# Performance work log

Measured on AMD Instinct MI355X. Metric: run time of the kernel, lower is better.

The kernel has to match this reference:

```python
import jax, jax.numpy as jnp
import numpy as np

# GNB per-element parameters [s, beta, R, C6] indexed by atomic number Z (rows not listed stay zero)
_ROWS = {
 1:[0.2772,1.7504,3.6516,95.99], 2:[0.2425,2.087,2.1843,40.67], 3:[0.3266,2.3073,1.2711,70.21],
 4:[0.3964,2.8811,3.3497,114.51], 5:[0.3121,2.6366,2.7079,152.36], 6:[0.2455,3.0189,1.8219,184.28],
 7:[0.2743,2.9432,2.4667,482.54], 8:[0.2577,2.7407,2.365,405.57], 9:[0.2791,2.5863,1.5062,218.45],
 10:[0.2378,2.5307,1.8233,174.81], 11:[0.2592,2.5679,1.3974,181.7], 12:[0.3837,2.9613,3.3515,263.02],
 13:[0.3013,3.2377,3.0102,228.1], 14:[0.3202,3.2749,3.1629,359.43], 15:[0.3399,3.7491,3.2554,3222.12],
 16:[0.3215,3.6718,2.9539,2144.49], 17:[0.3071,3.418,3.0368,2072.46], 18:[0.2752,3.3306,2.6598,1357.42],
 19:[0.2264,2.9736,4.0877,1406.65], 20:[0.4015,3.4464,4.1275,1058.36], 21:[0.9388,4.5955,9.7282,11498.73],
 22:[0.6048,3.5334,8.5322,3361.33], 23:[0.3678,3.068,7.2344,2095.91], 24:[0.2848,2.8393,5.3605,1049.31],
 25:[0.355,3.055,3.718,966.27], 26:[0.4406,3.2628,3.6408,1571.36], 27:[0.4124,3.2622,3.4961,1183.59],
 28:[0.3139,2.749,3.5108,787.76], 29:[0.3345,2.9097,3.0537,563.93], 30:[0.3391,2.9024,3.0261,592.91],
 31:[0.3146,3.3924,3.1735,430.82], 32:[0.3327,3.2804,3.1773,812.57], 33:[0.404,3.8757,3.8357,4533.53],
 34:[0.3343,3.8562,3.1109,3440.92], 35:[0.3242,3.7067,3.2122,3859.82], 36:[0.292,3.6457,2.8263,2729.6],
 37:[0.2677,3.4421,2.412,1864.19], 38:[0.3446,3.559,1.894,1175.73], 39:[1.0038,5.7293,11.2061,32141.18],
 40:[0.6146,5.075,6.821,27655.14], 41:[0.4244,3.7156,7.2367,2864.2], 42:[0.4882,3.6853,3.901,3563.45],
 43:[0.4439,3.6987,4.0857,3266.43], 44:[0.4736,3.7826,4.045,3967.23], 45:[0.4039,3.4706,3.4813,2233.82],
 46:[0.3188,3.3433,3.0487,1393.49], 47:[0.2948,3.1186,2.7795,1315.09], 48:[0.3012,3.0853,2.8673,1311.47],
 49:[0.3351,3.5452,3.3339,1460.56], 50:[0.3134,3.2997,3.0086,1662.99], 51:[0.4081,4.1277,3.9919,8089.97],
 52:[0.3585,4.1795,3.4209,6887.05], 53:[0.3574,4.0988,3.5649,8799.32], 54:[0.3134,4.0387,3.0288,6136.5],
 55:[0.2872,3.8468,2.262,3757.31], 56:[0.3788,4.0368,1.3837,2561.18], 57:[1.0851,6.1365,12.171,66580.83],
 72:[0.5577,5.213,6.0791,27593.76], 73:[0.5308,4.7637,5.7661,15364.65], 74:[0.3926,3.6018,3.6366,2734.5],
 75:[0.5351,3.9552,4.241,4801.82], 76:[0.4701,4.0278,4.1348,5685.94], 77:[0.3661,3.6123,3.4213,2786.0],
 78:[0.3411,3.6066,3.2486,2699.79], 79:[0.3164,3.3822,2.9588,2282.6], 80:[0.3047,3.375,2.9381,2476.79],
 81:[0.2802,3.3964,2.7711,2988.7], 82:[0.2682,3.2481,2.5816,2506.63], 83:[0.3876,4.1225,3.785,8916.84],
 84:[0.3679,4.2313,3.5381,8694.22], 85:[0.368,4.2455,3.6985,11821.61], 86:[0.3195,4.1784,3.0551,8410.64],
}
_TAB = np.zeros((87, 4), np.float32)
for _z, _v in _ROWS.items():
    _TAB[_z] = _v
GNB_TABLE = jnp.asarray(_TAB)
C_SP2 = jnp.asarray(np.array([0.2808, 3.0548, 2.2348, 429.69], np.float32))
C_SP3 = jnp.asarray(np.array([0.2455, 3.0189, 1.8219, 184.28], np.float32))
N_CN2 = jnp.asarray(np.array([0.2996, 3.02, 2.6454, 720.18], np.float32))
N_CN3 = jnp.asarray(np.array([0.2743, 2.9432, 2.4667, 482.54], np.float32))

BJ_A1, BJ_A2, BJ_ALPHA = 0.4, 4.0, 14.0
CUTOFF_LR, CUTOFF_START = 10.0, 8.0  # cutoff_start = cutoff_lr - 2.0


def _poly_envelope(x):
    # PolynomialCutoff.calculate_envelope with r_max=1, p=6:
    x6 = x ** 6
    env = 1.0 - 28.0 * x6 + 48.0 * x6 * x - 21.0 * x6 * x * x
    return env * (x < 1.0)


def _gnb_forward(lengths, Z, edge_index):
    n_nodes = Z.shape[0]
    sender, receiver = edge_index[0], edge_index[1]

    # coordination numbers via scatter-add on receiver
    cn = jnp.zeros((n_nodes,), jnp.int32).at[receiver].add(1)

    # species-indexed params with CN-adaptive selection for C and N
    params = GNB_TABLE[Z]  # [N, 4]
    c_params = jnp.where((cn <= 3)[:, None], C_SP2[None, :], C_SP3[None, :])
    n_params = jnp.where((cn <= 2)[:, None], N_CN2[None, :], N_CN3[None, :])
    params = jnp.where((Z == 6)[:, None], c_params, params)
    params = jnp.where((Z == 7)[:, None], n_params, params)

    R_i = params[:, 2]
    C6_i = params[:, 3]

    # geometric-mean combination rules per edge
    C6_ij = jnp.sqrt(C6_i[sender] * C6_i[receiver])
    R_ij = jnp.sqrt(R_i[sender] * R_i[receiver])

    r = lengths
    # BJ damping: f = 1 / (1 + 6 (r/r0)^(-alpha)), r0 = a1 sqrt(R_ij) + a2
    r0 = BJ_A1 * jnp.sqrt(R_ij) + BJ_A2
    f_damp = 1.0 / (1.0 + 6.0 * (r0 / r) ** BJ_ALPHA)

    e_edge = -C6_ij / (R_ij ** 6 + r ** 6) * f_damp

    # long-range polynomial cutoff switching from 1 at cutoff_start to 0 at cutoff_lr
    x = (r - CUTOFF_START) / (CUTOFF_LR - CUTOFF_START)
    env = jnp.where(r < CUTOFF_START, 1.0, _poly_envelope(x))
    e_edge = e_edge * env

    # scatter-sum to atoms; 0.5 to split symmetric pair energy over both directions
    node_energy = jnp.zeros((n_nodes,), e_edge.dtype).at[receiver].add(0.5 * e_edge)
    return node_energy


def setup_inputs() -> dict:
    key = jax.random.key(0)
    k1, k2, k3 = jax.random.split(key, 3)
    n_nodes, n_edges = 100000, 6400000
    Z = jax.random.randint(k1, (n_nodes,), 1, 87, dtype=jnp.int32)
    edge_index = jax.random.randint(k2, (2, n_edges), 0, n_nodes, dtype=jnp.int32)
    lengths = jax.random.uniform(k3, (n_edges,), jnp.float32, 1.0, 10.5)
    return {"Z": Z, "edge_index": edge_index, "lengths": lengths}


def reference(Z, edge_index, lengths):
    return _gnb_forward(lengths, Z, edge_index)
```

## Files before the change

### kernel.cpp

```cpp
#include <hip/hip_runtime.h>


#define B2SHIFT 10
#define B2SIZE  1024
#define TILE    4096
#define SBLK    512
#define ESLICES 32
#define MAXB    128
#define EB      256
#define AREP    4

__device__ __constant__ float2 GNB_RC6[87] = {
    {0.f, 0.f},
    {3.6516f, 95.99f},   {2.1843f, 40.67f},   {1.2711f, 70.21f},
    {3.3497f, 114.51f},  {2.7079f, 152.36f},  {1.8219f, 184.28f},
    {2.4667f, 482.54f},  {2.365f, 405.57f},   {1.5062f, 218.45f},
    {1.8233f, 174.81f},  {1.3974f, 181.7f},   {3.3515f, 263.02f},
    {3.0102f, 228.1f},   {3.1629f, 359.43f},  {3.2554f, 3222.12f},
    {2.9539f, 2144.49f}, {3.0368f, 2072.46f}, {2.6598f, 1357.42f},
    {4.0877f, 1406.65f}, {4.1275f, 1058.36f}, {9.7282f, 11498.73f},
    {8.5322f, 3361.33f}, {7.2344f, 2095.91f}, {5.3605f, 1049.31f},
    {3.718f, 966.27f},   {3.6408f, 1571.36f}, {3.4961f, 1183.59f},
    {3.5108f, 787.76f},  {3.0537f, 563.93f},  {3.0261f, 592.91f},
    {3.1735f, 430.82f},  {3.1773f, 812.57f},  {3.8357f, 4533.53f},
    {3.1109f, 3440.92f}, {3.2122f, 3859.82f}, {2.8263f, 2729.6f},
    {2.412f, 1864.19f},  {1.894f, 1175.73f},  {11.2061f, 32141.18f},
    {6.821f, 27655.14f}, {7.2367f, 2864.2f},  {3.901f, 3563.45f},
    {4.0857f, 3266.43f}, {4.045f, 3967.23f},  {3.4813f, 2233.82f},
    {3.0487f, 1393.49f}, {2.7795f, 1315.09f}, {2.8673f, 1311.47f},
    {3.3339f, 1460.56f}, {3.0086f, 1662.99f}, {3.9919f, 8089.97f},
    {3.4209f, 6887.05f}, {3.5649f, 8799.32f}, {3.0288f, 6136.5f},
    {2.262f, 3757.31f},  {1.3837f, 2561.18f}, {12.171f, 66580.83f},
    {0.f,0.f},{0.f,0.f},{0.f,0.f},{0.f,0.f},{0.f,0.f},{0.f,0.f},{0.f,0.f},
    {0.f,0.f},{0.f,0.f},{0.f,0.f},{0.f,0.f},{0.f,0.f},{0.f,0.f},{0.f,0.f},
    {6.0791f, 27593.76f}, {5.7661f, 15364.65f}, {3.6366f, 2734.5f},
    {4.241f, 4801.82f},   {4.1348f, 5685.94f},  {3.4213f, 2786.0f},
    {3.2486f, 2699.79f},  {2.9588f, 2282.6f},   {2.9381f, 2476.79f},
    {2.7711f, 2988.7f},   {2.5816f, 2506.63f},  {3.785f, 8916.84f},
    {3.5381f, 8694.22f},  {3.6985f, 11821.61f}, {3.0551f, 8410.64f},
};

__global__ void gnb_init(const int* __restrict__ Z, unsigned* __restrict__ isCN,
                         int nw, int n_nodes, int4* __restrict__ zp4, int zq,
                         int* __restrict__ zp, int zwords) {
    int stride = gridDim.x * blockDim.x;
    int t0 = blockIdx.x * blockDim.x + threadIdx.x;
    int4 z4 = make_int4(0, 0, 0, 0);
    for (int i = t0; i < zq; i += stride) zp4[i] = z4;
    for (int i = zq * 4 + t0; i < zwords; i += stride) zp[i] = 0;
    for (int w = t0; w < nw; w += stride) {
        unsigned m = 0;
        int base = w << 5;
        int lim = n_nodes - base; if (lim > 32) lim = 32;
        for (int k = 0; k < lim; ++k) {
            int z = Z[base + k];
            if (z == 6 || z == 7) m |= (1u << k);
        }
        isCN[w] = m;
    }
}

__global__ void __launch_bounds__(EB)
gnb_degree(const int* __restrict__ recv, const unsigned* __restrict__ isCN,
           int* __restrict__ cn, int n_edges) {
    int base = (blockIdx.x * EB + threadIdx.x) * 4;
    if (base + 3 < n_edges) {
        int4 rv = *(const int4*)(recv + base);
        int rr[4] = {rv.x, rv.y, rv.z, rv.w};
        #pragma unroll
        for (int j = 0; j < 4; ++j) {
            unsigned r = (unsigned)rr[j];
            if ((isCN[r >> 5] >> (r & 31)) & 1u) atomicAdd(&cn[r], 1);
        }
    } else {
        for (int j = 0; j < 4; ++j) {
            int e = base + j;
            if (e < n_edges) {
                unsigned r = (unsigned)recv[e];
                if ((isCN[r >> 5] >> (r & 31)) & 1u) atomicAdd(&cn[r], 1);
            }
        }
    }
}

__global__ void gnb_params(const int* __restrict__ Z, const int* __restrict__ cn,
                           float2* __restrict__ P2, int n_nodes) {
    int i = blockIdx.x * blockDim.x + threadIdx.x;
    if (i >= n_nodes) return;
    int z = Z[i];
    float Rp, C6;
    if (z == 6) {
        if (cn[i] <= 3) { Rp = 2.2348f; C6 = 429.69f; }
        else            { Rp = 1.8219f; C6 = 184.28f; }
    } else if (z == 7) {
        if (cn[i] <= 2) { Rp = 2.6454f; C6 = 720.18f; }
        else            { Rp = 2.4667f; C6 = 482.54f; }
    } else {
        float2 rc = GNB_RC6[z];
        Rp = rc.x; C6 = rc.y;
    }
    P2[i] = make_float2(sqrtf(C6), sqrtf(sqrtf(Rp)));
}

__device__ __forceinline__ float gnb_energy_eval(float2 ps, float2 pr, float rlen) {
    float env;
    if (rlen < 8.0f) {
        env = 1.0f;
    } else {
        float x = (rlen - 8.0f) * 0.5f;
        float x2 = x * x;
        float x6 = x2 * x2 * x2;
        env = 1.0f - 28.0f * x6 + 48.0f * x6 * x - 21.0f * x6 * x2;
    }
    float sR  = ps.y * pr.y;
    float C6  = ps.x * pr.x;
    float Rij = sR * sR;
    float R3  = Rij * Rij * Rij;
    float R6  = R3 * R3;
    float r0  = 0.4f * sR + 4.0f;
    float t   = r0 / rlen;
    float t2 = t * t, t4 = t2 * t2, t8 = t4 * t4;
    float t14 = t8 * t4 * t2;
    float fd = 1.0f / (1.0f + 6.0f * t14);
    float rl2 = rlen * rlen;
    float r6 = rl2 * rl2 * rl2;
    return -0.5f * C6 / (R6 + r6) * fd * env;
}

__global__ void __launch_bounds__(SBLK)
gnb_scatter(const int* __restrict__ send, const int* __restrict__ recv,
            const float* __restrict__ len, const float2* __restrict__ P2,
            unsigned* __restrict__ buckets, unsigned* __restrict__ cursor,
            uint2* __restrict__ ovrec, unsigned* __restrict__ ocur,
            int n_edges, unsigned cap, unsigned ocap) {
    __shared__ unsigned hist[MAXB];
    __shared__ unsigned gbase[MAXB];
    const int tid = threadIdx.x;
    const int e0  = blockIdx.x * TILE;

    if (tid < MAXB) hist[tid] = 0;
    __syncthreads();

    unsigned pk[2][4];
    unsigned bk[2][4];
    const bool full = (e0 + TILE <= n_edges);
    #pragma unroll
    for (int k = 0; k < 2; ++k) {
        int base = e0 + (k * SBLK + tid) * 4;
        int ss[4]; int rr[4]; float ll[4];
        if (full) {
            int4   sv = *(const int4*)(send + base);
            int4   rv = *(const int4*)(recv + base);
            float4 lv = *(const float4*)(len + base);
            ss[0]=sv.x; ss[1]=sv.y; ss[2]=sv.z; ss[3]=sv.w;
            rr[0]=rv.x; rr[1]=rv.y; rr[2]=rv.z; rr[3]=rv.w;
            ll[0]=lv.x; ll[1]=lv.y; ll[2]=lv.z; ll[3]=lv.w;
        } else {
            for (int j = 0; j < 4; ++j) {
                int e = base + j;
                bool ok = (e < n_edges);
                ss[j] = ok ? send[e] : 0;
                rr[j] = ok ? recv[e] : 0;
                ll[j] = ok ? len[e]  : 1.0e9f;
            }
        }
        #pragma unroll
        for (int j = 0; j < 4; ++j) {
            if (ll[j] < 10.0f) {
                float e = gnb_energy_eval(P2[ss[j]], P2[rr[j]], ll[j]);
                unsigned eb = (__float_as_uint(e) + 512u) & ~1023u;
                unsigned r  = (unsigned)rr[j];
                unsigned b  = r >> B2SHIFT;
                unsigned off = atomicAdd(&hist[b], 1u);
                pk[k][j] = eb | (r & (B2SIZE - 1));
                bk[k][j] = b | (off << 7);
            } else {
                bk[k][j] = 0xFFFFFFFFu;
            }
        }
    }
    __syncthreads();

    if (tid < MAXB) {
        unsigned c = hist[tid];
        gbase[tid] = c ? atomicAdd(&cursor[tid], c) : 0u;
    }
    __syncthreads();

    #pragma unroll
    for (int k = 0; k < 2; ++k) {
        #pragma unroll
        for (int j = 0; j < 4; ++j) {
            unsigned bo = bk[k][j];
            if (bo != 0xFFFFFFFFu) {
                unsigned b = bo & (MAXB - 1);
                unsigned g = gbase[b] + (bo >> 7);
                if (g < cap) {
                    buckets[(size_t)b * cap + g] = pk[k][j];
                } else {
                    unsigned o = atomicAdd(ocur, 1u);
                    if (o < ocap)
                        ovrec[o] = make_uint2((b << B2SHIFT) | (pk[k][j] & (B2SIZE - 1)),
                                              pk[k][j] & ~1023u);
                }
            }
        }
    }
}

__global__ void __launch_bounds__(256)
gnb_accum(const unsigned* __restrict__ buckets, const unsigned* __restrict__ cursor,
          const uint2* __restrict__ ovrec, const unsigned* __restrict__ ocur,
          float* __restrict__ rep, unsigned cap, unsigned ocap) {
    __shared__ float acc[AREP][B2SIZE + 8];
    const int b   = blockIdx.x / ESLICES;
    const int sl  = blockIdx.x % ESLICES;
    const int tid = threadIdx.x;
    const int rr  = (tid >> 6) & (AREP - 1);

    for (int i = tid; i < AREP * (B2SIZE + 8); i += 256) acc[0][i] = 0.0f;
    __syncthreads();

    unsigned count = cursor[b];
    if (count > cap) count = cap;
    unsigned seg = (((count + ESLICES - 1) / ESLICES) + 3u) & ~3u;
    unsigned st  = (unsigned)sl * seg; if (st > count) st = count;
    unsigned en  = st + seg; if (en > count) en = count;

    const unsigned* src = buckets + (size_t)b * cap;
    for (unsigned i = st + tid * 4; i < en; i += 1024) {
        if (i + 4 <= en) {
            uint4 v = *(const uint4*)(src + i);
            atomicAdd(&acc[rr][v.x & (B2SIZE - 1)], __uint_as_float(v.x & ~1023u));
            atomicAdd(&acc[rr][v.y & (B2SIZE - 1)], __uint_as_float(v.y & ~1023u));
            atomicAdd(&acc[rr][v.z & (B2SIZE - 1)], __uint_as_float(v.z & ~1023u));
            atomicAdd(&acc[rr][v.w & (B2SIZE - 1)], __uint_as_float(v.w & ~1023u));
        } else {
            for (unsigned t = i; t < en; ++t) {
                unsigned v = src[t];
                atomicAdd(&acc[rr][v & (B2SIZE - 1)], __uint_as_float(v & ~1023u));
            }
        }
    }

    if (sl == 0) {
        unsigned n = *ocur; if (n > ocap) n = ocap;
        for (unsigned i = tid; i < n; i += 256) {
            uint2 rc = ovrec[i];
            if ((rc.x >> B2SHIFT) == (unsigned)b)
                atomicAdd(&acc[rr][rc.x & (B2SIZE - 1)], __uint_as_float(rc.y));
        }
    }
    __syncthreads();

    float* dst = rep + (size_t)blockIdx.x * B2SIZE;
    for (int i = tid; i < B2SIZE; i += 256)
        dst[i] = (acc[0][i] + acc[1][i]) + (acc[2][i] + acc[3][i]);
}

__global__ void gnb_reduce(const float* __restrict__ rep, float* __restrict__ out,
                           int n_nodes) {
    int i = blockIdx.x * blockDim.x + threadIdx.x;
    if (i >= n_nodes) return;
    int b = i >> B2SHIFT;
    int j = i & (B2SIZE - 1);
    const float* src = rep + ((size_t)b * ESLICES) * B2SIZE + j;
    float sum = 0.0f;
    #pragma unroll
    for (int s = 0; s < ESLICES; ++s) sum += src[(size_t)s * B2SIZE];
    out[i] = sum;
}

extern "C" void kernel_launch(void* const* d_in, const int* in_sizes, int n_in,
                              void* d_out, int out_size, void* d_ws, size_t ws_size,
                              hipStream_t stream) {
    const int*   Z    = (const int*)d_in[0];
    const int*   eidx = (const int*)d_in[1];
    const float* len  = (const float*)d_in[2];
    float*       out  = (float*)d_out;

    const int n_nodes = in_sizes[0];
    const int n_edges = in_sizes[2];
    const int* send = eidx;
    const int* recv = eidx + n_edges;

    const int NB2 = (n_nodes + B2SIZE - 1) >> B2SHIFT;
    const int nw  = (n_nodes + 31) >> 5;
    const int nwp = (nw + 7) & ~7;

    char* ws = (char*)d_ws;
    unsigned* cursor = (unsigned*)ws;
    unsigned* ocur   = (unsigned*)(ws + MAXB * 4);
    int*      cn     = (int*)(ws + (MAXB + 8) * 4);
    float2*   P2     = (float2*)(ws + ((size_t)n_nodes + MAXB + 8) * 4);
    unsigned* isCN   = (unsigned*)(ws + ((size_t)3 * n_nodes + MAXB + 8) * 4);
    float*    rep    = (float*)((char*)isCN + (size_t)nwp * 4);
    size_t rep_w     = (size_t)NB2 * ESLICES * B2SIZE;
    char*     tail   = (char*)rep + rep_w * 4;

    size_t fixed_words = (size_t)3 * n_nodes + MAXB + 8 + nwp + rep_w;
    size_t total_words = ws_size / 4;
    size_t avail = total_words > fixed_words ? total_words - fixed_words : 0;
    size_t ovw = avail / 64;
    unsigned ocap = (unsigned)((ovw / 2) & ~1ull);
    size_t capw = (avail - ovw) / (size_t)NB2;
    capw &= ~(size_t)3;
    long cap = (long)capw;
    if (cap > n_edges) cap = (n_edges + 3) & ~3;
    if (cap < 0) cap = 0;
    uint2*    ovrec   = (uint2*)tail;
    unsigned* buckets = (unsigned*)(tail + (size_t)ocap * 8);

    const int B = 256;
    int node_blocks = (n_nodes + B - 1) / B;
    int edge4_blocks = (n_edges + EB * 4 - 1) / (EB * 4);
    int scat_blocks = (n_edges + TILE - 1) / TILE;
    int zero_words  = n_nodes + MAXB + 8;
    int zq = zero_words / 4;

    gnb_init<<<256, B, 0, stream>>>(Z, isCN, nw, n_nodes, (int4*)ws, zq,
                                    (int*)ws, zero_words);
    gnb_degree<<<edge4_blocks, EB, 0, stream>>>(recv, isCN, cn, n_edges);
    gnb_params<<<node_blocks, B, 0, stream>>>(Z, cn, P2, n_nodes);
    gnb_scatter<<<scat_blocks, SBLK, 0, stream>>>(send, recv, len, P2, buckets,
                                                  cursor, ovrec, ocur, n_edges,
                                                  (unsigned)cap, ocap);
    gnb_accum<<<NB2 * ESLICES, B, 0, stream>>>(buckets, cursor, ovrec, ocur,
                                               rep, (unsigned)cap, ocap);
    gnb_reduce<<<node_blocks, B, 0, stream>>>(rep, out, n_nodes);
}
```

Before: 232.2 us.

## Batch parameter gathers and defer energy eval past histogram barrier; reduce accum slices

The scatter kernel now loads all eight edges' index and length data up front and issues all sixteen parameter gathers together. It builds the shared-memory histogram first and computes the energies between the global cursor atomic and the barrier, so that math overlaps atomic latency. The receiver's low bits are packed into the bucket key so the packed record is built only at write time. Separately, the accumulate kernel uses fewer edge slices per bucket (8 instead of 32), which means fewer blocks and fewer replica flushes but less parallelism. The bit packing assumes the per-block offset fits in the top bits; with 4096 edges per tile it needs 13 bits, and 15 are available.

```diff
diff --git a/kernel.cpp b/kernel.cpp
--- a/kernel.cpp
+++ b/kernel.cpp
@@ -5,7 +5,7 @@
 #define B2SIZE  1024
 #define TILE    4096
 #define SBLK    512
-#define ESLICES 32
+#define ESLICES 8
 #define MAXB    128
 #define EB      256
 #define AREP    4
@@ -141,42 +141,45 @@
     if (tid < MAXB) hist[tid] = 0;
     __syncthreads();
 
-    unsigned pk[2][4];
-    unsigned bk[2][4];
+    int ss[8]; unsigned rr[8]; float ll[8];
     const bool full = (e0 + TILE <= n_edges);
-    #pragma unroll
-    for (int k = 0; k < 2; ++k) {
-        int base = e0 + (k * SBLK + tid) * 4;
-        int ss[4]; int rr[4]; float ll[4];
-        if (full) {
-            int4   sv = *(const int4*)(send + base);
-            int4   rv = *(const int4*)(recv + base);
-            float4 lv = *(const float4*)(len + base);
-            ss[0]=sv.x; ss[1]=sv.y; ss[2]=sv.z; ss[3]=sv.w;
-            rr[0]=rv.x; rr[1]=rv.y; rr[2]=rv.z; rr[3]=rv.w;
-            ll[0]=lv.x; ll[1]=lv.y; ll[2]=lv.z; ll[3]=lv.w;
+    if (full) {
+        int4   sv0 = *(const int4*)(send + e0 + tid * 4);
+        int4   rv0 = *(const int4*)(recv + e0 + tid * 4);
+        float4 lv0 = *(const float4*)(len + e0 + tid * 4);
+        int4   sv1 = *(const int4*)(send + e0 + 2048 + tid * 4);
+        int4   rv1 = *(const int4*)(recv + e0 + 2048 + tid * 4);
+        float4 lv1 = *(const float4*)(len + e0 + 2048 + tid * 4);
+        ss[0]=sv0.x; ss[1]=sv0.y; ss[2]=sv0.z; ss[3]=sv0.w;
+        ss[4]=sv1.x; ss[5]=sv1.y; ss[6]=sv1.z; ss[7]=sv1.w;
+        rr[0]=(unsigned)rv0.x; rr[1]=(unsigned)rv0.y; rr[2]=(unsigned)rv0.z; rr[3]=(unsigned)rv0.w;
+        rr[4]=(unsigned)rv1.x; rr[5]=(unsigned)rv1.y; rr[6]=(unsigned)rv1.z; rr[7]=(unsigned)rv1.w;
+        ll[0]=lv0.x; ll[1]=lv0.y; ll[2]=lv0.z; ll[3]=lv0.w;
+        ll[4]=lv1.x; ll[5]=lv1.y; ll[6]=lv1.z; ll[7]=lv1.w;
+    } else {
+        #pragma unroll
+        for (int i = 0; i < 8; ++i) {
+            int e = e0 + ((i >> 2) * 2048) + tid * 4 + (i & 3);
+            bool ok = (e < n_edges);
+            ss[i] = ok ? send[e] : 0;
+            rr[i] = ok ? (unsigned)recv[e] : 0u;
+            ll[i] = ok ? len[e] : 1.0e9f;
+        }
+    }
+
+    float2 Ps[8], Pr[8];
+    #pragma unroll
+    for (int i = 0; i < 8; ++i) { Ps[i] = P2[ss[i]]; Pr[i] = P2[rr[i]]; }
+
+    unsigned bk[8];
+    #pragma unroll
+    for (int i = 0; i < 8; ++i) {
+        if (ll[i] < 10.0f) {
+            unsigned b   = rr[i] >> B2SHIFT;
+            unsigned off = atomicAdd(&hist[b], 1u);
+            bk[i] = b | ((rr[i] & (B2SIZE - 1)) << 7) | (off << 17);
         } else {
-            for (int j = 0; j < 4; ++j) {
-                int e = base + j;
-                bool ok = (e < n_edges);
-                ss[j] = ok ? send[e] : 0;
-                rr[j] = ok ? recv[e] : 0;
-                ll[j] = ok ? len[e]  : 1.0e9f;
-            }
-        }
-        #pragma unroll
-        for (int j = 0; j < 4; ++j) {
-            if (ll[j] < 10.0f) {
-                float e = gnb_energy_eval(P2[ss[j]], P2[rr[j]], ll[j]);
-                unsigned eb = (__float_as_uint(e) + 512u) & ~1023u;
-                unsigned r  = (unsigned)rr[j];
-                unsigned b  = r >> B2SHIFT;
-                unsigned off = atomicAdd(&hist[b], 1u);
-                pk[k][j] = eb | (r & (B2SIZE - 1));
-                bk[k][j] = b | (off << 7);
-            } else {
-                bk[k][j] = 0xFFFFFFFFu;
-            }
+            bk[i] = 0x80000000u;
         }
     }
     __syncthreads();
@@ -185,24 +188,24 @@
         unsigned c = hist[tid];
         gbase[tid] = c ? atomicAdd(&cursor[tid], c) : 0u;
     }
-    __syncthreads();
-
-    #pragma unroll
-    for (int k = 0; k < 2; ++k) {
-        #pragma unroll
-        for (int j = 0; j < 4; ++j) {
-            unsigned bo = bk[k][j];
-            if (bo != 0xFFFFFFFFu) {
-                unsigned b = bo & (MAXB - 1);
-                unsigned g = gbase[b] + (bo >> 7);
-                if (g < cap) {
-                    buckets[(size_t)b * cap + g] = pk[k][j];
-                } else {
-                    unsigned o = atomicAdd(ocur, 1u);
-                    if (o < ocap)
-                        ovrec[o] = make_uint2((b << B2SHIFT) | (pk[k][j] & (B2SIZE - 1)),
-                                              pk[k][j] & ~1023u);
-                }
+    float ev[8];
+    #pragma unroll
+    for (int i = 0; i < 8; ++i) ev[i] = gnb_energy_eval(Ps[i], Pr[i], ll[i]);
+    __syncthreads();
+
+    #pragma unroll
+    for (int i = 0; i < 8; ++i) {
+        unsigned bo = bk[i];
+        if (!(bo & 0x80000000u)) {
+            unsigned b    = bo & (MAXB - 1);
+            unsigned rlow = (bo >> 7) & (B2SIZE - 1);
+            unsigned g    = gbase[b] + (bo >> 17);
+            unsigned eb   = (__float_as_uint(ev[i]) + 512u) & ~1023u;
+            if (g < cap) {
+                buckets[(size_t)b * cap + g] = eb | rlow;
+            } else {
+                unsigned o = atomicAdd(ocur, 1u);
+                if (o < ocap) ovrec[o] = make_uint2((b << B2SHIFT) | rlow, eb);
             }
         }
     }
```

Measured after the change: 240.0 us. 3.3% more time.
